# Kernel tuning notes

Hardware: AMD Instinct MI355X
Metric: run time of the kernel (lower is better)

## Reference

```python
import jax, jax.numpy as jnp
import numpy as np

NUM_TOKENS = 16384
INPUT_DIM = 4096
NUM_EXPERTS = 64
TOPK = 2


def setup_inputs() -> dict:
    key = jax.random.key(0)
    k1, k2 = jax.random.split(key)
    tokens = jax.random.normal(k1, (NUM_TOKENS, INPUT_DIM), dtype=jnp.float32)
    # nn.Linear(input_dim, num_experts).weight has shape [num_experts, input_dim]
    W = jax.random.normal(k2, (NUM_EXPERTS, INPUT_DIM), dtype=jnp.float32) * (1.0 / np.sqrt(INPUT_DIM))
    return {"tokens": tokens, "W": W}


def reference(tokens, W):
    # logits: [num_tokens, num_experts] = tokens @ W.T
    logits = jnp.einsum("td,ed->te", tokens, W)
    scores = jax.nn.softmax(logits, axis=-1)
    topk_scores, topk_indices = jax.lax.top_k(scores, TOPK)
    return topk_scores, topk_indices
```

## Files before the change

kernel.cpp:

```cpp
#include <hip/hip_runtime.h>
#include <math.h>

#define NTOK 16384
#define DIM  4096
#define NEXP 64
#define KS   2
#define KSL  (DIM / KS)
#define BK   64
#define NCH  (KSL / BK)
#define BM   64
#define KSF  4

typedef __fp16 f16x8  __attribute__((ext_vector_type(8)));
typedef __fp16 f16x2  __attribute__((ext_vector_type(2)));
typedef float  f32x16 __attribute__((ext_vector_type(16)));

__device__ __forceinline__ void gl_lds16(const void* g, void* l) {
  __builtin_amdgcn_global_load_lds(
      (const __attribute__((address_space(1))) void*)g,
      (__attribute__((address_space(3))) void*)l, 16, 0, 0);
}

__global__ __launch_bounds__(256) void split_w(
    const float* __restrict__ W,
    __fp16* __restrict__ Wh,
    __fp16* __restrict__ Wl)
{
  const int i = blockIdx.x * 256 + threadIdx.x;
  const float w = W[i];
  const __fp16 h = (__fp16)w;
  const float r = w - (float)h;
  Wh[i] = h;
  Wl[i] = (__fp16)r;
}

__global__ __launch_bounds__(512, 2) void router_mfma(
    const float* __restrict__ tokens,
    const __fp16* __restrict__ Wh,
    const __fp16* __restrict__ Wl,
    float* __restrict__ partial)
{
  __shared__ float  As[2][BM * BK];
  __shared__ __fp16 Bh[2][NEXP * BK];
  __shared__ __fp16 Bl[2][NEXP * BK];

  const int tid  = threadIdx.x;
  const int wid  = tid >> 6;
  const int lane = tid & 63;
  const int rc2  = lane & 31;
  const int q2   = lane >> 5;
  const int kh   = wid & 1;
  const int ec   = (wid >> 1) & 1;
  const int wr   = wid >> 2;
  const int s    = blockIdx.x & (KS - 1);
  const int tb   = (blockIdx.x >> 1) * BM;
  const int kbase = s * KSL;

  const int r4 = lane >> 4, aj = lane & 15;
  const int ra0 = 8 * wid + r4;
  const int ra1 = 8 * wid + 4 + r4;
  const float* asrc0 = tokens + (size_t)(tb + ra0) * DIM + kbase
                       + ((aj ^ (ra0 & 15)) << 2);
  const float* asrc1 = tokens + (size_t)(tb + ra1) * DIM + kbase
                       + ((aj ^ (ra1 & 15)) << 2);
  const int e8 = lane >> 3, bj = lane & 7;
  const int rb = 8 * wid + e8;
  const size_t boff = (size_t)rb * DIM + kbase + ((bj ^ (rb & 7)) << 3);
  const __fp16* bsrc_h = Wh + boff;
  const __fp16* bsrc_l = Wl + boff;

#define STAGE(buf, c) {                                   \
    const int ko = (c) * BK;                              \
    gl_lds16(asrc0 + ko, &As[buf][(8 * wid) * BK]);       \
    gl_lds16(asrc1 + ko, &As[buf][(8 * wid + 4) * BK]);   \
    gl_lds16(bsrc_h + ko, &Bh[buf][(8 * wid) * BK]);      \
    gl_lds16(bsrc_l + ko, &Bl[buf][(8 * wid) * BK]);      \
  }

  f32x16 acc = {0,0,0,0, 0,0,0,0, 0,0,0,0, 0,0,0,0};

  const int akey = rc2 & 15;
  const int bkey = rc2 & 7;
  const int Arow = (32 * wr + rc2) * BK;
  const int Brow = (32 * ec + rc2) * BK;

#define KSTEP(buf, kk) {                                                     \
    const int ks_ = 2 * kh + (kk);                                           \
    const int u0 = 4 * ks_ + 2 * q2;                                         \
    const float4 a0 = *(const float4*)(&As[buf][Arow + ((u0    ) ^ akey) * 4]); \
    const float4 a1 = *(const float4*)(&As[buf][Arow + ((u0 + 1) ^ akey) * 4]); \
    const int ub = ((2 * ks_ + q2) ^ bkey) * 8;                              \
    const f16x8 bhv = *(const f16x8*)(&Bh[buf][Brow + ub]);                  \
    const f16x8 blv = *(const f16x8*)(&Bl[buf][Brow + ub]);                  \
    const f16x2 h0 = __builtin_amdgcn_cvt_pkrtz(a0.x, a0.y);                 \
    const f16x2 h1 = __builtin_amdgcn_cvt_pkrtz(a0.z, a0.w);                 \
    const f16x2 h2 = __builtin_amdgcn_cvt_pkrtz(a1.x, a1.y);                 \
    const f16x2 h3 = __builtin_amdgcn_cvt_pkrtz(a1.z, a1.w);                 \
    const f16x2 m0 = __builtin_amdgcn_cvt_pkrtz(a0.x - (float)h0[0],         \
                                                a0.y - (float)h0[1]);        \
    const f16x2 m1 = __builtin_amdgcn_cvt_pkrtz(a0.z - (float)h1[0],         \
                                                a0.w - (float)h1[1]);        \
    const f16x2 m2 = __builtin_amdgcn_cvt_pkrtz(a1.x - (float)h2[0],         \
                                                a1.y - (float)h2[1]);        \
    const f16x2 m3 = __builtin_amdgcn_cvt_pkrtz(a1.z - (float)h3[0],         \
                                                a1.w - (float)h3[1]);        \
    const f16x8 Ah = {h0[0],h0[1],h1[0],h1[1],h2[0],h2[1],h3[0],h3[1]};      \
    const f16x8 Am = {m0[0],m0[1],m1[0],m1[1],m2[0],m2[1],m3[0],m3[1]};      \
    acc = __builtin_amdgcn_mfma_f32_32x32x16_f16(Ah, bhv, acc, 0, 0, 0);     \
    acc = __builtin_amdgcn_mfma_f32_32x32x16_f16(Ah, blv, acc, 0, 0, 0);     \
    acc = __builtin_amdgcn_mfma_f32_32x32x16_f16(Am, bhv, acc, 0, 0, 0);     \
  }

#define COMP(buf) { KSTEP(buf, 0); KSTEP(buf, 1); }

  STAGE(0, 0);
  __syncthreads();

  for (int c = 0; c < NCH; c += 2) {
    if (c + 1 < NCH) STAGE(1, c + 1);
    COMP(0);
    __syncthreads();
    if (c + 2 < NCH) STAGE(0, c + 2);
    COMP(1);
    __syncthreads();
  }
#undef STAGE
#undef COMP
#undef KSTEP

  float* P = partial + ((size_t)(2 * s + kh) * NTOK + tb + 32 * wr) * NEXP
             + 32 * ec;
  #pragma unroll
  for (int reg = 0; reg < 16; ++reg) {
    const int row = (reg & 3) + 8 * (reg >> 2) + 4 * q2;
    P[(size_t)row * NEXP + rc2] = acc[reg];
  }
}

__global__ __launch_bounds__(256) void router_finish(
    const float* __restrict__ partial,
    float* __restrict__ out)
{
  const int t = blockIdx.x * 256 + threadIdx.x;

  float l[NEXP];
  const float* p0 = partial + (size_t)t * NEXP;
  #pragma unroll
  for (int qq = 0; qq < 16; ++qq) {
    const float4 v = *(const float4*)(p0 + qq * 4);
    l[qq*4+0] = v.x; l[qq*4+1] = v.y; l[qq*4+2] = v.z; l[qq*4+3] = v.w;
  }
  #pragma unroll
  for (int s = 1; s < KSF; ++s) {
    const float* p = partial + ((size_t)s * NTOK + t) * NEXP;
    #pragma unroll
    for (int qq = 0; qq < 16; ++qq) {
      const float4 v = *(const float4*)(p + qq * 4);
      l[qq*4+0] += v.x; l[qq*4+1] += v.y; l[qq*4+2] += v.z; l[qq*4+3] += v.w;
    }
  }

  float t1v = l[0]; int t1i = 0;
  float t2v = -INFINITY; int t2i = NEXP;
  #pragma unroll
  for (int e = 1; e < NEXP; ++e) {
    const float v = l[e];
    if (v > t1v) { t2v = t1v; t2i = t1i; t1v = v; t1i = e; }
    else if (v > t2v) { t2v = v; t2i = e; }
  }

  float ssum = 0.f;
  #pragma unroll
  for (int e = 0; e < NEXP; ++e) ssum += expf(l[e] - t1v);

  const float inv = 1.0f / ssum;
  out[t * 2 + 0] = inv;
  out[t * 2 + 1] = expf(t2v - t1v) * inv;
  out[2 * NTOK + t * 2 + 0] = (float)t1i;
  out[2 * NTOK + t * 2 + 1] = (float)t2i;
}

extern "C" void kernel_launch(void* const* d_in, const int* in_sizes, int n_in,
                              void* d_out, int out_size, void* d_ws, size_t ws_size,
                              hipStream_t stream) {
  const float* tokens = (const float*)d_in[0];
  const float* W      = (const float*)d_in[1];
  float* out          = (float*)d_out;

  __fp16* Wh = (__fp16*)d_ws;
  __fp16* Wl = Wh + (size_t)NEXP * DIM;
  float* partial = (float*)((char*)d_ws + (size_t)2 * NEXP * DIM * sizeof(__fp16));

  split_w<<<(NEXP * DIM) / 256, 256, 0, stream>>>(W, Wh, Wl);
  router_mfma<<<(NTOK / BM) * KS, 512, 0, stream>>>(tokens, Wh, Wl, partial);
  router_finish<<<NTOK / 256, 256, 0, stream>>>(partial, out);
}
```

Before: 75.12 us.

## Drop K-split, triple-buffer LDS with vmcnt waits, vectorize weight split

Removes the two-way K split so each block walks the full K dimension, which halves the partial-sum traffic and the reduction work in the finish kernel. The main loop becomes a three-stage LDS ring that uses explicit s_waitcnt vmcnt and raw barriers in place of __syncthreads, so loads are issued two chunks ahead. The weight split kernel is vectorized to float4. In exchange there are only 256 blocks at one block per CU, which lowers occupancy and parallelism on the GPU.

```diff
diff --git a/kernel.cpp b/kernel.cpp
--- a/kernel.cpp
+++ b/kernel.cpp
@@ -4,14 +4,13 @@
 #define NTOK 16384
 #define DIM  4096
 #define NEXP 64
-#define KS   2
-#define KSL  (DIM / KS)
 #define BK   64
-#define NCH  (KSL / BK)
+#define NCH  (DIM / BK)
 #define BM   64
-#define KSF  4
+#define KSF  2
 
 typedef __fp16 f16x8  __attribute__((ext_vector_type(8)));
+typedef __fp16 f16x4  __attribute__((ext_vector_type(4)));
 typedef __fp16 f16x2  __attribute__((ext_vector_type(2)));
 typedef float  f32x16 __attribute__((ext_vector_type(16)));
 
@@ -26,23 +25,27 @@
     __fp16* __restrict__ Wh,
     __fp16* __restrict__ Wl)
 {
-  const int i = blockIdx.x * 256 + threadIdx.x;
-  const float w = W[i];
-  const __fp16 h = (__fp16)w;
-  const float r = w - (float)h;
-  Wh[i] = h;
-  Wl[i] = (__fp16)r;
+  const int i = (blockIdx.x * 256 + threadIdx.x) * 4;
+  const float4 w = *(const float4*)(W + i);
+  f16x4 h, l;
+  h[0] = (__fp16)w.x; h[1] = (__fp16)w.y; h[2] = (__fp16)w.z; h[3] = (__fp16)w.w;
+  l[0] = (__fp16)(w.x - (float)h[0]);
+  l[1] = (__fp16)(w.y - (float)h[1]);
+  l[2] = (__fp16)(w.z - (float)h[2]);
+  l[3] = (__fp16)(w.w - (float)h[3]);
+  *(f16x4*)(Wh + i) = h;
+  *(f16x4*)(Wl + i) = l;
 }
 
-__global__ __launch_bounds__(512, 2) void router_mfma(
+__global__ __launch_bounds__(512, 1) void router_mfma(
     const float* __restrict__ tokens,
     const __fp16* __restrict__ Wh,
     const __fp16* __restrict__ Wl,
     float* __restrict__ partial)
 {
-  __shared__ float  As[2][BM * BK];
-  __shared__ __fp16 Bh[2][NEXP * BK];
-  __shared__ __fp16 Bl[2][NEXP * BK];
+  __shared__ float  As[3][BM * BK];
+  __shared__ __fp16 Bh[3][NEXP * BK];
+  __shared__ __fp16 Bl[3][NEXP * BK];
 
   const int tid  = threadIdx.x;
   const int wid  = tid >> 6;
@@ -52,24 +55,20 @@
   const int kh   = wid & 1;
   const int ec   = (wid >> 1) & 1;
   const int wr   = wid >> 2;
-  const int s    = blockIdx.x & (KS - 1);
-  const int tb   = (blockIdx.x >> 1) * BM;
-  const int kbase = s * KSL;
+  const int tb   = blockIdx.x * BM;
 
   const int r4 = lane >> 4, aj = lane & 15;
   const int ra0 = 8 * wid + r4;
   const int ra1 = 8 * wid + 4 + r4;
-  const float* asrc0 = tokens + (size_t)(tb + ra0) * DIM + kbase
-                       + ((aj ^ (ra0 & 15)) << 2);
-  const float* asrc1 = tokens + (size_t)(tb + ra1) * DIM + kbase
-                       + ((aj ^ (ra1 & 15)) << 2);
+  const float* asrc0 = tokens + (size_t)(tb + ra0) * DIM + ((aj ^ (ra0 & 15)) << 2);
+  const float* asrc1 = tokens + (size_t)(tb + ra1) * DIM + ((aj ^ (ra1 & 15)) << 2);
   const int e8 = lane >> 3, bj = lane & 7;
   const int rb = 8 * wid + e8;
-  const size_t boff = (size_t)rb * DIM + kbase + ((bj ^ (rb & 7)) << 3);
+  const size_t boff = (size_t)rb * DIM + ((bj ^ (rb & 7)) << 3);
   const __fp16* bsrc_h = Wh + boff;
   const __fp16* bsrc_l = Wl + boff;
 
-#define STAGE(buf, c) {                                   \
+#define STAGE(buf, c) if ((c) < NCH) {                    \
     const int ko = (c) * BK;                              \
     gl_lds16(asrc0 + ko, &As[buf][(8 * wid) * BK]);       \
     gl_lds16(asrc1 + ko, &As[buf][(8 * wid + 4) * BK]);   \
@@ -113,23 +112,27 @@
 
 #define COMP(buf) { KSTEP(buf, 0); KSTEP(buf, 1); }
 
+#define VM(n) asm volatile("s_waitcnt vmcnt(" #n ")" ::: "memory")
+#define BAR() __builtin_amdgcn_s_barrier()
+
   STAGE(0, 0);
-  __syncthreads();
+  STAGE(1, 1);
 
-  for (int c = 0; c < NCH; c += 2) {
-    if (c + 1 < NCH) STAGE(1, c + 1);
-    COMP(0);
-    __syncthreads();
-    if (c + 2 < NCH) STAGE(0, c + 2);
-    COMP(1);
-    __syncthreads();
+  for (int i = 0; i < 21; ++i) {
+    const int c = 3 * i;
+    VM(4); BAR(); STAGE(2, c + 2); COMP(0);
+    VM(4); BAR(); STAGE(0, c + 3); COMP(1);
+    VM(4); BAR(); STAGE(1, c + 4); COMP(2);
   }
+  VM(0); BAR(); COMP(0);
+
 #undef STAGE
 #undef COMP
 #undef KSTEP
+#undef VM
+#undef BAR
 
-  float* P = partial + ((size_t)(2 * s + kh) * NTOK + tb + 32 * wr) * NEXP
-             + 32 * ec;
+  float* P = partial + ((size_t)kh * NTOK + tb + 32 * wr) * NEXP + 32 * ec;
   #pragma unroll
   for (int reg = 0; reg < 16; ++reg) {
     const int row = (reg & 3) + 8 * (reg >> 2) + 4 * q2;
@@ -145,19 +148,13 @@
 
   float l[NEXP];
   const float* p0 = partial + (size_t)t * NEXP;
+  const float* p1 = partial + ((size_t)NTOK + t) * NEXP;
   #pragma unroll
   for (int qq = 0; qq < 16; ++qq) {
-    const float4 v = *(const float4*)(p0 + qq * 4);
-    l[qq*4+0] = v.x; l[qq*4+1] = v.y; l[qq*4+2] = v.z; l[qq*4+3] = v.w;
-  }
-  #pragma unroll
-  for (int s = 1; s < KSF; ++s) {
-    const float* p = partial + ((size_t)s * NTOK + t) * NEXP;
-    #pragma unroll
-    for (int qq = 0; qq < 16; ++qq) {
-      const float4 v = *(const float4*)(p + qq * 4);
-      l[qq*4+0] += v.x; l[qq*4+1] += v.y; l[qq*4+2] += v.z; l[qq*4+3] += v.w;
-    }
+    const float4 v0 = *(const float4*)(p0 + qq * 4);
+    const float4 v1 = *(const float4*)(p1 + qq * 4);
+    l[qq*4+0] = v0.x + v1.x; l[qq*4+1] = v0.y + v1.y;
+    l[qq*4+2] = v0.z + v1.z; l[qq*4+3] = v0.w + v1.w;
   }
 
   float t1v = l[0]; int t1i = 0;
@@ -191,7 +188,7 @@
   __fp16* Wl = Wh + (size_t)NEXP * DIM;
   float* partial = (float*)((char*)d_ws + (size_t)2 * NEXP * DIM * sizeof(__fp16));
 
-  split_w<<<(NEXP * DIM) / 256, 256, 0, stream>>>(W, Wh, Wl);
-  router_mfma<<<(NTOK / BM) * KS, 512, 0, stream>>>(tokens, Wh, Wl, partial);
+  split_w<<<(NEXP * DIM) / 1024, 256, 0, stream>>>(W, Wh, Wl);
+  router_mfma<<<NTOK / BM, 512, 0, stream>>>(tokens, Wh, Wl, partial);
   router_finish<<<NTOK / 256, 256, 0, stream>>>(partial, out);
 }
```

New measurement: 93.07 us. 1.24x slower.
